# Kernel tuning notes

Hardware: AMD Instinct MI355X
Metric: run time of the kernel (lower is better)

The kernel has to match this reference:

```python
import jax, jax.numpy as jnp
import numpy as np

EPS = 1e-05


def setup_inputs() -> dict:
    key = jax.random.key(0)
    kx, = jax.random.split(key, 1)
    B, C, T = 8, 512, 8192
    x = jax.random.normal(kx, (B, C, T), dtype=jnp.float32)
    weight = jnp.ones((1, C, 1), dtype=jnp.float32)
    bias = jnp.zeros((1, C, 1), dtype=jnp.float32)
    return {"x": x, "weight": weight, "bias": bias}


def reference(x, weight, bias):
    # x: [B, C, T]; causal (running) per-channel mean/var over time.
    T = x.shape[-1]
    count = jnp.arange(1, T + 1, dtype=x.dtype)  # [T], broadcasts over B,C
    cumsum = jnp.cumsum(x, axis=-1)
    cumsum_sq = jnp.cumsum(x * x, axis=-1)
    mean = cumsum / count
    var = cumsum_sq / count - mean * mean
    x_norm = (x - mean) * jax.lax.rsqrt(var + EPS)
    return x_norm * weight + bias
```

## Files before the change

### kernel.cpp

```cpp
#include <hip/hip_runtime.h>
#include <math.h>

#define EPS 1e-5f

__global__ __launch_bounds__(256) void causal_ln_kernel(
    const float* __restrict__ x,
    const float* __restrict__ weight,
    const float* __restrict__ bias,
    float* __restrict__ out,
    int C, int T)
{
    const int row  = blockIdx.x;
    const int c    = row % C;
    const float wv = weight[c];
    const float bv = bias[c];
    const long long base = (long long)row * (long long)T;

    const int t     = threadIdx.x;
    const int lane  = t & 63;
    const int wid   = t >> 6;
    const int chunk = t * 32;

    const float4* xp = (const float4*)(x + base + chunk);
    float4 v[8];
#pragma unroll
    for (int j = 0; j < 8; ++j) v[j] = xp[j];

    float s = 0.f, s2 = 0.f;
#pragma unroll
    for (int j = 0; j < 8; ++j) {
        s  += v[j].x + v[j].y + v[j].z + v[j].w;
        s2 += v[j].x * v[j].x + v[j].y * v[j].y
            + v[j].z * v[j].z + v[j].w * v[j].w;
    }

    float ws = s, ws2 = s2;
#pragma unroll
    for (int off = 1; off < 64; off <<= 1) {
        float a  = __shfl_up(ws,  off, 64);
        float a2 = __shfl_up(ws2, off, 64);
        if (lane >= off) { ws += a; ws2 += a2; }
    }

    __shared__ float wsum[4], wsum2[4];
    if (lane == 63) { wsum[wid] = ws; wsum2[wid] = ws2; }
    __syncthreads();
    float off1 = 0.f, off2 = 0.f;
#pragma unroll
    for (int k = 0; k < 4; ++k) {
        if (k < wid) { off1 += wsum[k]; off2 += wsum2[k]; }
    }

    float es  = __shfl_up(ws,  1, 64);
    float es2 = __shfl_up(ws2, 1, 64);
    if (lane == 0) { es = 0.f; es2 = 0.f; }
    float run  = off1 + es;
    float run2 = off2 + es2;

    float cnt = (float)chunk;
#pragma unroll
    for (int j = 0; j < 8; ++j) {
        float xs[4] = {v[j].x, v[j].y, v[j].z, v[j].w};
#pragma unroll
        for (int i = 0; i < 4; ++i) {
            float xi = xs[i];
            run  += xi;
            run2 += xi * xi;
            cnt  += 1.f;
            float rc   = __builtin_amdgcn_rcpf(cnt);
            float mean = run * rc;
            float var  = run2 * rc - mean * mean;
            var = fmaxf(var, 0.f);
            float rinv = __builtin_amdgcn_rsqf(var + EPS);
            xs[i] = (xi - mean) * rinv * wv + bv;
        }
        v[j] = make_float4(xs[0], xs[1], xs[2], xs[3]);
    }

    float4* op = (float4*)(out + base + chunk);
#pragma unroll
    for (int j = 0; j < 8; ++j) op[j] = v[j];
}

extern "C" void kernel_launch(void* const* d_in, const int* in_sizes, int n_in,
                              void* d_out, int out_size, void* d_ws, size_t ws_size,
                              hipStream_t stream) {
    const float* x      = (const float*)d_in[0];
    const float* weight = (const float*)d_in[1];
    const float* bias   = (const float*)d_in[2];
    float* out          = (float*)d_out;

    const int C = in_sizes[1];
    const int T = 8192;
    const int rows = in_sizes[0] / T;

    dim3 grid(rows), block(256);
    hipLaunchKernelGGL(causal_ln_kernel, grid, block, 0, stream,
                       x, weight, bias, out, C, T);
}
```

Baseline: 246.8 us.

## Stage row through padded LDS for coalesced global loads and stores

Global loads and stores now use a coalesced pattern where consecutive threads touch consecutive float4s. Data is transposed through a padded shared-memory buffer (stride 36) so each thread still works on its own 32-element contiguous chunk for the scan. Before, each thread read 128 contiguous bytes, so accesses across a wavefront were strided. The cost is about 36 KB of LDS per block, which may reduce occupancy, plus extra barriers and LDS traffic.

```diff
diff --git a/kernel.cpp b/kernel.cpp
--- a/kernel.cpp
+++ b/kernel.cpp
@@ -10,21 +10,34 @@
     float* __restrict__ out,
     int C, int T)
 {
+    __shared__ float lds[256 * 36];
+    __shared__ float wsum[4], wsum2[4];
+
     const int row  = blockIdx.x;
     const int c    = row % C;
     const float wv = weight[c];
     const float bv = bias[c];
     const long long base = (long long)row * (long long)T;
 
-    const int t     = threadIdx.x;
-    const int lane  = t & 63;
-    const int wid   = t >> 6;
-    const int chunk = t * 32;
+    const int t    = threadIdx.x;
+    const int lane = t & 63;
+    const int wid  = t >> 6;
 
-    const float4* xp = (const float4*)(x + base + chunk);
+    const float4* xg = (const float4*)(x + base);
+#pragma unroll
+    for (int j = 0; j < 8; ++j) {
+        int g = j * 256 + t;
+        float4 f = xg[g];
+        int owner  = g >> 3;
+        int within = g & 7;
+        *(float4*)&lds[owner * 36 + within * 4] = f;
+    }
+    __syncthreads();
+
     float4 v[8];
 #pragma unroll
-    for (int j = 0; j < 8; ++j) v[j] = xp[j];
+    for (int j = 0; j < 8; ++j)
+        v[j] = *(const float4*)&lds[t * 36 + j * 4];
 
     float s = 0.f, s2 = 0.f;
 #pragma unroll
@@ -42,7 +55,6 @@
         if (lane >= off) { ws += a; ws2 += a2; }
     }
 
-    __shared__ float wsum[4], wsum2[4];
     if (lane == 63) { wsum[wid] = ws; wsum2[wid] = ws2; }
     __syncthreads();
     float off1 = 0.f, off2 = 0.f;
@@ -57,7 +69,7 @@
     float run  = off1 + es;
     float run2 = off2 + es2;
 
-    float cnt = (float)chunk;
+    float cnt = (float)(t * 32);
 #pragma unroll
     for (int j = 0; j < 8; ++j) {
         float xs[4] = {v[j].x, v[j].y, v[j].z, v[j].w};
@@ -74,12 +86,18 @@
             float rinv = __builtin_amdgcn_rsqf(var + EPS);
             xs[i] = (xi - mean) * rinv * wv + bv;
         }
-        v[j] = make_float4(xs[0], xs[1], xs[2], xs[3]);
+        *(float4*)&lds[t * 36 + j * 4] = make_float4(xs[0], xs[1], xs[2], xs[3]);
     }
+    __syncthreads();
 
-    float4* op = (float4*)(out + base + chunk);
+    float4* og = (float4*)(out + base);
 #pragma unroll
-    for (int j = 0; j < 8; ++j) op[j] = v[j];
+    for (int j = 0; j < 8; ++j) {
+        int g = j * 256 + t;
+        int owner  = g >> 3;
+        int within = g & 7;
+        og[g] = *(const float4*)&lds[owner * 36 + within * 4];
+    }
 }
 
 extern "C" void kernel_launch(void* const* d_in, const int* in_sizes, int n_in,
```

After: 232.8 us. -5.7%, faster.

## Interleave row segments across threads for coalesced loads with multi-segment scan

Applied to the files above, without the earlier changes.

Each thread now handles four interleaved float4 segments, so every load and store instruction is contiguous across the block instead of strided by 128 bytes. The block doubles to 512 threads and runs a separate wave and block prefix scan per segment, then combines segment totals. Output uses nontemporal stores. The trade is more shuffle and LDS scan work per row.

```diff
diff --git a/kernel.cpp b/kernel.cpp
--- a/kernel.cpp
+++ b/kernel.cpp
@@ -2,64 +2,88 @@
 #include <math.h>
 
 #define EPS 1e-5f
+#define TPB 512
+#define NJ  4
 
-__global__ __launch_bounds__(256) void causal_ln_kernel(
+typedef float f32x4 __attribute__((ext_vector_type(4)));
+
+__global__ __launch_bounds__(TPB, 6) void causal_ln_kernel(
     const float* __restrict__ x,
     const float* __restrict__ weight,
     const float* __restrict__ bias,
     float* __restrict__ out,
     int C, int T)
 {
+    __shared__ float wt [NJ][8];
+    __shared__ float wt2[NJ][8];
+
     const int row  = blockIdx.x;
     const int c    = row % C;
     const float wv = weight[c];
     const float bv = bias[c];
     const long long base = (long long)row * (long long)T;
 
-    const int t     = threadIdx.x;
-    const int lane  = t & 63;
-    const int wid   = t >> 6;
-    const int chunk = t * 32;
+    const int t    = threadIdx.x;
+    const int lane = t & 63;
+    const int wid  = t >> 6;
 
-    const float4* xp = (const float4*)(x + base + chunk);
-    float4 v[8];
+    const f32x4* xg = (const f32x4*)(x + base);
+    f32x4 v[NJ];
 #pragma unroll
-    for (int j = 0; j < 8; ++j) v[j] = xp[j];
+    for (int j = 0; j < NJ; ++j) v[j] = xg[j * TPB + t];
 
-    float s = 0.f, s2 = 0.f;
+    float s[NJ], s2[NJ];
 #pragma unroll
-    for (int j = 0; j < 8; ++j) {
-        s  += v[j].x + v[j].y + v[j].z + v[j].w;
-        s2 += v[j].x * v[j].x + v[j].y * v[j].y
-            + v[j].z * v[j].z + v[j].w * v[j].w;
+    for (int j = 0; j < NJ; ++j) {
+        s [j] = v[j].x + v[j].y + v[j].z + v[j].w;
+        s2[j] = v[j].x * v[j].x + v[j].y * v[j].y
+              + v[j].z * v[j].z + v[j].w * v[j].w;
     }
 
-    float ws = s, ws2 = s2;
+    float ws[NJ], ws2[NJ];
+#pragma unroll
+    for (int j = 0; j < NJ; ++j) { ws[j] = s[j]; ws2[j] = s2[j]; }
 #pragma unroll
     for (int off = 1; off < 64; off <<= 1) {
-        float a  = __shfl_up(ws,  off, 64);
-        float a2 = __shfl_up(ws2, off, 64);
-        if (lane >= off) { ws += a; ws2 += a2; }
+#pragma unroll
+        for (int j = 0; j < NJ; ++j) {
+            float a  = __shfl_up(ws [j], off, 64);
+            float a2 = __shfl_up(ws2[j], off, 64);
+            ws [j] += (lane >= off) ? a  : 0.f;
+            ws2[j] += (lane >= off) ? a2 : 0.f;
+        }
     }
 
-    __shared__ float wsum[4], wsum2[4];
-    if (lane == 63) { wsum[wid] = ws; wsum2[wid] = ws2; }
+    if (lane == 63) {
+#pragma unroll
+        for (int j = 0; j < NJ; ++j) { wt[j][wid] = ws[j]; wt2[j][wid] = ws2[j]; }
+    }
     __syncthreads();
-    float off1 = 0.f, off2 = 0.f;
+
+    float start[NJ], start2[NJ];
+    {
+        float jpre = 0.f, jpre2 = 0.f;
 #pragma unroll
-    for (int k = 0; k < 4; ++k) {
-        if (k < wid) { off1 += wsum[k]; off2 += wsum2[k]; }
+        for (int j = 0; j < NJ; ++j) {
+            float wpre = 0.f, wpre2 = 0.f, btot = 0.f, btot2 = 0.f;
+#pragma unroll
+            for (int w = 0; w < 8; ++w) {
+                float a = wt[j][w], a2 = wt2[j][w];
+                btot  += a;  btot2 += a2;
+                wpre  += (w < wid) ? a  : 0.f;
+                wpre2 += (w < wid) ? a2 : 0.f;
+            }
+            start [j] = jpre  + wpre  + (ws [j] - s [j]);
+            start2[j] = jpre2 + wpre2 + (ws2[j] - s2[j]);
+            jpre  += btot;  jpre2 += btot2;
+        }
     }
 
-    float es  = __shfl_up(ws,  1, 64);
-    float es2 = __shfl_up(ws2, 1, 64);
-    if (lane == 0) { es = 0.f; es2 = 0.f; }
-    float run  = off1 + es;
-    float run2 = off2 + es2;
-
-    float cnt = (float)chunk;
 #pragma unroll
-    for (int j = 0; j < 8; ++j) {
+    for (int j = 0; j < NJ; ++j) {
+        float run  = start [j];
+        float run2 = start2[j];
+        float cnt  = (float)(j * (TPB * 4) + t * 4);
         float xs[4] = {v[j].x, v[j].y, v[j].z, v[j].w};
 #pragma unroll
         for (int i = 0; i < 4; ++i) {
@@ -74,12 +98,14 @@
             float rinv = __builtin_amdgcn_rsqf(var + EPS);
             xs[i] = (xi - mean) * rinv * wv + bv;
         }
-        v[j] = make_float4(xs[0], xs[1], xs[2], xs[3]);
+        f32x4 r = {xs[0], xs[1], xs[2], xs[3]};
+        v[j] = r;
     }
 
-    float4* op = (float4*)(out + base + chunk);
+    f32x4* og = (f32x4*)(out + base);
 #pragma unroll
-    for (int j = 0; j < 8; ++j) op[j] = v[j];
+    for (int j = 0; j < NJ; ++j)
+        __builtin_nontemporal_store(v[j], &og[j * TPB + t]);
 }
 
 extern "C" void kernel_launch(void* const* d_in, const int* in_sizes, int n_in,
@@ -94,7 +120,7 @@
     const int T = 8192;
     const int rows = in_sizes[0] / T;
 
-    dim3 grid(rows), block(256);
+    dim3 grid(rows), block(TPB);
     hipLaunchKernelGGL(causal_ln_kernel, grid, block, 0, stream,
                        x, weight, bias, out, C, T);
 }
```

Result: faster. 237.6 us (-3.7%).
